# Kernel optimization log

Hardware: AMD Instinct MI355X
Metric: run time of the kernel (lower is better)

## Reference

```python
import jax, jax.numpy as jnp
import numpy as np

D_MODEL = 1024
N_HEADS = 16
D_HEAD = D_MODEL // N_HEADS


def setup_inputs() -> dict:
    key = jax.random.key(0)
    ks = jax.random.split(key, 11)
    B, S = 4, 2048
    scale = 1.0 / np.sqrt(D_MODEL)
    inp = {
        "query": jax.random.normal(ks[0], (B, S, D_MODEL), jnp.float32),
        "key": jax.random.normal(ks[1], (B, S, D_MODEL), jnp.float32),
        "value": jax.random.normal(ks[2], (B, S, D_MODEL), jnp.float32),
        "Wq": jax.random.normal(ks[3], (D_MODEL, D_MODEL), jnp.float32) * scale,
        "bq": jnp.zeros((D_MODEL,), jnp.float32),
        "Wk": jax.random.normal(ks[4], (D_MODEL, D_MODEL), jnp.float32) * scale,
        "bk": jnp.zeros((D_MODEL,), jnp.float32),
        "Wv": jax.random.normal(ks[5], (D_MODEL, D_MODEL), jnp.float32) * scale,
        "bv": jnp.zeros((D_MODEL,), jnp.float32),
        "Wo": jax.random.normal(ks[6], (D_MODEL, D_MODEL), jnp.float32) * scale,
        "bo": jnp.zeros((D_MODEL,), jnp.float32),
    }
    return inp


def _split_heads(x):
    b, s, _ = x.shape
    return x.reshape(b, s, N_HEADS, D_HEAD).transpose(0, 2, 1, 3)  # [b,h,s,dh]


def reference(query, key, value, Wq, bq, Wk, bk, Wv, bv, Wo, bo):
    Q = _split_heads(query @ Wq + bq)
    K = _split_heads(key @ Wk + bk)
    V = _split_heads(value @ Wv + bv)
    scores = jnp.einsum("bhqd,bhkd->bhqk", Q, K) / jnp.sqrt(jnp.float32(D_HEAD))
    attn = jax.nn.softmax(scores, axis=-1)  # dropout p=0 (eval)
    context = jnp.einsum("bhqk,bhkd->bhqd", attn, V)
    b, h, s, dh = context.shape
    context = context.transpose(0, 2, 1, 3).reshape(b, s, D_MODEL)
    return context @ Wo + bo
```

## Files before the change

kernel.cpp:

```cpp
#include <hip/hip_runtime.h>
#include <stdint.h>

#define DM 1024
#define SEQ 2048
#define MTOT 8192

typedef __attribute__((ext_vector_type(8))) short bf16x8;
typedef __attribute__((ext_vector_type(4))) float f32x4;
typedef __attribute__((ext_vector_type(16))) float f32x16;
typedef __attribute__((ext_vector_type(8))) unsigned short u16x8;
typedef __attribute__((ext_vector_type(4))) unsigned short u16x4;
typedef __attribute__((ext_vector_type(4))) uint32_t u32x4;
typedef __attribute__((ext_vector_type(2))) unsigned int u32x2;

__device__ __forceinline__ unsigned short f2bf(float x) {
  uint32_t u = __builtin_bit_cast(uint32_t, x);
  u += 0x7fffu + ((u >> 16) & 1u);
  return (unsigned short)(u >> 16);
}

__device__ __forceinline__ uint32_t cvtpk_bf16(float lo, float hi) {
  uint32_t r;
  asm("v_cvt_pk_bf16_f32 %0, %1, %2" : "=v"(r) : "v"(lo), "v"(hi));
  return r;
}

__device__ __forceinline__ void gload16(void* lds, const void* g) {
  __builtin_amdgcn_global_load_lds(
      (const __attribute__((address_space(1))) void*)(uintptr_t)g,
      (__attribute__((address_space(3))) void*)(uintptr_t)lds,
      16, 0, 0);
}

__global__ __launch_bounds__(256)
void prep_w(const float* __restrict__ w0, const float* __restrict__ w1,
            const float* __restrict__ w2, const float* __restrict__ w3,
            unsigned short* __restrict__ Wt) {
  const int z = blockIdx.z;
  const float* W = z == 0 ? w0 : z == 1 ? w1 : z == 2 ? w2 : w3;
  unsigned short* out = Wt + (size_t)z * 1048576;
  __shared__ float tile[32][33];
  const int n0 = blockIdx.x * 32, k0 = blockIdx.y * 32;
  const int tx = threadIdx.x & 31, ty = threadIdx.x >> 5;
#pragma unroll
  for (int j = 0; j < 32; j += 8)
    tile[ty + j][tx] = W[(size_t)(k0 + ty + j) * DM + n0 + tx];
  __syncthreads();
#pragma unroll
  for (int j = 0; j < 32; j += 8)
    out[(size_t)(n0 + ty + j) * DM + k0 + tx] = f2bf(tile[tx][ty + j]);
}

__global__ __launch_bounds__(256)
void cvt3(const float* __restrict__ q, const float* __restrict__ k,
          const float* __restrict__ v, unsigned short* __restrict__ out) {
  const int z = blockIdx.y;
  const float* in = z == 0 ? q : z == 1 ? k : v;
  unsigned short* o = out + (size_t)z * MTOT * DM;
  int i = blockIdx.x * 256 + threadIdx.x;
  f32x4 a = *(const f32x4*)(in + (size_t)i * 8);
  f32x4 b = *(const f32x4*)(in + (size_t)i * 8 + 4);
  u16x8 ov;
#pragma unroll
  for (int j = 0; j < 4; ++j) { ov[j] = f2bf(a[j]); ov[4 + j] = f2bf(b[j]); }
  *(u16x8*)(o + (size_t)i * 8) = ov;
}

template <int MODE>
__global__ __launch_bounds__(256)
void gemm_bt(const unsigned short* __restrict__ A,
             const unsigned short* __restrict__ Wt,
             const float* __restrict__ bias,
             void* __restrict__ C, float oscale) {
  __shared__ char sA[16384];
  __shared__ char sB[16384];
  const int t = threadIdx.x, wave = t >> 6, lane = t & 63;
  const int m0 = blockIdx.x * 128, n0 = blockIdx.y * 128;
  const int wr = (wave >> 1) * 64, wc = (wave & 1) * 64;
  const int lr = lane & 15, kg = lane >> 4;

  f32x4 acc[4][4];
#pragma unroll
  for (int i = 0; i < 4; ++i)
#pragma unroll
    for (int j = 0; j < 4; ++j) acc[i][j] = (f32x4){0.f, 0.f, 0.f, 0.f};

  for (int kt = 0; kt < 16; ++kt) {
    __syncthreads();
#pragma unroll
    for (int i = 0; i < 4; ++i) {
      int c = wave * 4 + i;
      int row = c * 8 + (lane >> 3);
      int bo = ((lane & 7) * 16) ^ ((row & 7) << 4);
      gload16(&sA[c * 1024], (const char*)(A + (size_t)(m0 + row) * DM + kt * 64) + bo);
      gload16(&sB[c * 1024], (const char*)(Wt + (size_t)(n0 + row) * DM + kt * 64) + bo);
    }
    __syncthreads();
#pragma unroll
    for (int ks = 0; ks < 2; ++ks) {
      bf16x8 afr[4], bfr[4];
#pragma unroll
      for (int j = 0; j < 4; ++j) {
        int mr = wr + j * 16 + lr;
        afr[j] = *(const bf16x8*)&sA[mr * 128 + ((ks * 64 + kg * 16) ^ ((mr & 7) << 4))];
        int nr = wc + j * 16 + lr;
        bfr[j] = *(const bf16x8*)&sB[nr * 128 + ((ks * 64 + kg * 16) ^ ((nr & 7) << 4))];
      }
#pragma unroll
      for (int mi = 0; mi < 4; ++mi)
#pragma unroll
        for (int nj = 0; nj < 4; ++nj)
          acc[mi][nj] = __builtin_amdgcn_mfma_f32_16x16x32_bf16(afr[mi], bfr[nj], acc[mi][nj], 0, 0, 0);
    }
  }
#pragma unroll
  for (int nj = 0; nj < 4; ++nj) {
    int col = n0 + wc + nj * 16 + lr;
    float bv = bias[col];
#pragma unroll
    for (int mi = 0; mi < 4; ++mi) {
      int rowseq = m0 + wr + mi * 16 + kg * 4;
      if (MODE == 2) {
        u16x4 pk;
#pragma unroll
        for (int r = 0; r < 4; ++r) pk[r] = f2bf(acc[mi][nj][r] + bv);
        *(u16x4*)((unsigned short*)C +
                  ((size_t)((rowseq >> 11) << 10) + col) * SEQ + (rowseq & 2047)) = pk;
      } else {
#pragma unroll
        for (int r = 0; r < 4; ++r) {
          float v = (acc[mi][nj][r] + bv) * oscale;
          if (MODE == 1) ((float*)C)[(size_t)(rowseq + r) * DM + col] = v;
          else ((unsigned short*)C)[(size_t)(rowseq + r) * DM + col] = f2bf(v);
        }
      }
    }
  }
}

__global__ __launch_bounds__(256)
void gemm_qkv(const unsigned short* __restrict__ Xall,
              const unsigned short* __restrict__ Wt,
              const float* __restrict__ bq, const float* __restrict__ bk,
              const float* __restrict__ bv,
              unsigned short* __restrict__ Qb, unsigned short* __restrict__ Kb,
              unsigned short* __restrict__ Vt, float qscale) {
  __shared__ char sA[16384];
  __shared__ char sB[16384];
  const int z = blockIdx.z;
  const unsigned short* A = Xall + (size_t)z * MTOT * DM;
  const unsigned short* W = Wt + (size_t)z * 1048576;
  const float* bias = z == 0 ? bq : z == 1 ? bk : bv;
  const int t = threadIdx.x, wave = t >> 6, lane = t & 63;
  const int m0 = blockIdx.x * 128, n0 = blockIdx.y * 128;
  const int wr = (wave >> 1) * 64, wc = (wave & 1) * 64;
  const int lr = lane & 15, kg = lane >> 4;

  f32x4 acc[4][4];
#pragma unroll
  for (int i = 0; i < 4; ++i)
#pragma unroll
    for (int j = 0; j < 4; ++j) acc[i][j] = (f32x4){0.f, 0.f, 0.f, 0.f};

  for (int kt = 0; kt < 16; ++kt) {
    __syncthreads();
#pragma unroll
    for (int i = 0; i < 4; ++i) {
      int c = wave * 4 + i;
      int row = c * 8 + (lane >> 3);
      int bo = ((lane & 7) * 16) ^ ((row & 7) << 4);
      gload16(&sA[c * 1024], (const char*)(A + (size_t)(m0 + row) * DM + kt * 64) + bo);
      gload16(&sB[c * 1024], (const char*)(W + (size_t)(n0 + row) * DM + kt * 64) + bo);
    }
    __syncthreads();
#pragma unroll
    for (int ks = 0; ks < 2; ++ks) {
      bf16x8 afr[4], bfr[4];
#pragma unroll
      for (int j = 0; j < 4; ++j) {
        int mr = wr + j * 16 + lr;
        afr[j] = *(const bf16x8*)&sA[mr * 128 + ((ks * 64 + kg * 16) ^ ((mr & 7) << 4))];
        int nr = wc + j * 16 + lr;
        bfr[j] = *(const bf16x8*)&sB[nr * 128 + ((ks * 64 + kg * 16) ^ ((nr & 7) << 4))];
      }
#pragma unroll
      for (int mi = 0; mi < 4; ++mi)
#pragma unroll
        for (int nj = 0; nj < 4; ++nj)
          acc[mi][nj] = __builtin_amdgcn_mfma_f32_16x16x32_bf16(afr[mi], bfr[nj], acc[mi][nj], 0, 0, 0);
    }
  }
  const float sc = z == 0 ? qscale : 1.0f;
#pragma unroll
  for (int nj = 0; nj < 4; ++nj) {
    int col = n0 + wc + nj * 16 + lr;
    float bvv = bias[col];
#pragma unroll
    for (int mi = 0; mi < 4; ++mi) {
      int rowseq = m0 + wr + mi * 16 + kg * 4;
      if (z == 2) {
        u16x4 pk;
#pragma unroll
        for (int r = 0; r < 4; ++r) pk[r] = f2bf(acc[mi][nj][r] + bvv);
        *(u16x4*)(Vt + ((size_t)((rowseq >> 11) << 10) + col) * SEQ + (rowseq & 2047)) = pk;
      } else {
        unsigned short* out = z == 0 ? Qb : Kb;
#pragma unroll
        for (int r = 0; r < 4; ++r)
          out[(size_t)(rowseq + r) * DM + col] = f2bf((acc[mi][nj][r] + bvv) * sc);
      }
    }
  }
}

__global__ __launch_bounds__(512)
void attn(const unsigned short* __restrict__ Qb,
          const unsigned short* __restrict__ Kb,
          const unsigned short* __restrict__ Vt,
          unsigned short* __restrict__ Ctx) {
  __shared__ char sK[4][8192];
  __shared__ char sV[4][8192];
  const int t = threadIdx.x, wave = t >> 6, lane = t & 63;
  const int l31 = lane & 31, hi = lane >> 5;
  const int bh = blockIdx.x, b = bh >> 4, h = bh & 15;
  const int q0 = blockIdx.y * 512;

  const int srow = wave * 8 + (lane >> 3);
  const int sbo = ((lane & 7) * 16) ^ ((srow & 7) << 4);
  const char* gK = (const char*)Kb + ((size_t)b * SEQ + srow) * (DM * 2) + h * 128 + sbo;
  const char* gV = (const char*)Vt + ((size_t)bh * 64 + srow) * (SEQ * 2) + sbo;

#define STAGE1(buf, kt) do { \
    gload16(&sK[buf][wave * 1024], gK + (size_t)(kt) * 131072); \
    gload16(&sV[buf][wave * 1024], gV + (size_t)(kt) * 128); \
  } while (0)

  bf16x8 qfA[4], qfB[4];
  {
    const unsigned short* qpA = Qb + ((size_t)b * SEQ + q0 + wave * 64 + l31) * DM + h * 64 + hi * 8;
    const unsigned short* qpB = qpA + (size_t)32 * DM;
#pragma unroll
    for (int ks = 0; ks < 4; ++ks) {
      qfA[ks] = *(const bf16x8*)(qpA + ks * 16);
      qfB[ks] = *(const bf16x8*)(qpB + ks * 16);
    }
  }

  f32x16 oA0, oA1, oB0, oB1, mInit;
#pragma unroll
  for (int i = 0; i < 16; ++i) {
    oA0[i] = 0.f; oA1[i] = 0.f; oB0[i] = 0.f; oB1[i] = 0.f; mInit[i] = -12.0f;
  }
  float lA = 0.f, lB = 0.f;

  STAGE1(0, 0);
  STAGE1(1, 1);
  __syncthreads();

  for (int p = 0; p < SEQ / 128; ++p) {
    if (p + 1 < SEQ / 128) {
      const int nt = 2 * p + 2;
      STAGE1(nt & 3, nt);
      STAGE1((nt + 1) & 3, nt + 1);
    }
#pragma unroll
    for (int half = 0; half < 2; ++half) {
      const int buf = 2 * (p & 1) + half;

      f32x16 sA0 = mInit, sA1 = mInit, sB0 = mInit, sB1 = mInit;
      const char* kbase = sK[buf];
      __builtin_amdgcn_s_setprio(1);
#pragma unroll
      for (int ks = 0; ks < 4; ++ks) {
        const int swz = (ks * 32 + hi * 16) ^ ((l31 & 7) << 4);
        bf16x8 kf0 = *(const bf16x8*)(kbase + l31 * 128 + swz);
        bf16x8 kf1 = *(const bf16x8*)(kbase + (32 + l31) * 128 + swz);
        sA0 = __builtin_amdgcn_mfma_f32_32x32x16_bf16(kf0, qfA[ks], sA0, 0, 0, 0);
        sB0 = __builtin_amdgcn_mfma_f32_32x32x16_bf16(kf0, qfB[ks], sB0, 0, 0, 0);
        sA1 = __builtin_amdgcn_mfma_f32_32x32x16_bf16(kf1, qfA[ks], sA1, 0, 0, 0);
        sB1 = __builtin_amdgcn_mfma_f32_32x32x16_bf16(kf1, qfB[ks], sB1, 0, 0, 0);
      }
      __builtin_amdgcn_s_setprio(0);

      {
        float a0 = 0.f, a1 = 0.f, b0 = 0.f, b1 = 0.f;
#pragma unroll
        for (int i = 0; i < 16; i += 2) {
          float pa0 = __builtin_amdgcn_exp2f(sA0[i + 0]); sA0[i + 0] = pa0; a0 += pa0;
          float pa1 = __builtin_amdgcn_exp2f(sA0[i + 1]); sA0[i + 1] = pa1; a1 += pa1;
          float pb0 = __builtin_amdgcn_exp2f(sB0[i + 0]); sB0[i + 0] = pb0; b0 += pb0;
          float pb1 = __builtin_amdgcn_exp2f(sB0[i + 1]); sB0[i + 1] = pb1; b1 += pb1;
        }
#pragma unroll
        for (int i = 0; i < 16; i += 2) {
          float pa0 = __builtin_amdgcn_exp2f(sA1[i + 0]); sA1[i + 0] = pa0; a0 += pa0;
          float pa1 = __builtin_amdgcn_exp2f(sA1[i + 1]); sA1[i + 1] = pa1; a1 += pa1;
          float pb0 = __builtin_amdgcn_exp2f(sB1[i + 0]); sB1[i + 0] = pb0; b0 += pb0;
          float pb1 = __builtin_amdgcn_exp2f(sB1[i + 1]); sB1[i + 1] = pb1; b1 += pb1;
        }
        lA += a0 + a1;
        lB += b0 + b1;
      }

      const char* vbase = sV[buf];
#pragma unroll
      for (int sl = 0; sl < 4; ++sl) {
        const f32x16& spA = (sl < 2) ? sA0 : sA1;
        const f32x16& spB = (sl < 2) ? sB0 : sB1;
        const int s8 = (sl & 1) * 8;
        uint32_t ax0 = cvtpk_bf16(spA[s8 + 0], spA[s8 + 1]);
        uint32_t ax1 = cvtpk_bf16(spA[s8 + 2], spA[s8 + 3]);
        uint32_t ay0 = cvtpk_bf16(spA[s8 + 4], spA[s8 + 5]);
        uint32_t ay1 = cvtpk_bf16(spA[s8 + 6], spA[s8 + 7]);
        u32x2 ra0 = __builtin_amdgcn_permlane32_swap(ax0, ay0, false, false);
        u32x2 ra1 = __builtin_amdgcn_permlane32_swap(ax1, ay1, false, false);
        u32x4 wvA;
        wvA[0] = ra0[0];
        wvA[1] = ra1[0];
        wvA[2] = ra0[1];
        wvA[3] = ra1[1];
        bf16x8 pfA = __builtin_bit_cast(bf16x8, wvA);
        uint32_t bx0 = cvtpk_bf16(spB[s8 + 0], spB[s8 + 1]);
        uint32_t bx1 = cvtpk_bf16(spB[s8 + 2], spB[s8 + 3]);
        uint32_t by0 = cvtpk_bf16(spB[s8 + 4], spB[s8 + 5]);
        uint32_t by1 = cvtpk_bf16(spB[s8 + 6], spB[s8 + 7]);
        u32x2 rb0 = __builtin_amdgcn_permlane32_swap(bx0, by0, false, false);
        u32x2 rb1 = __builtin_amdgcn_permlane32_swap(bx1, by1, false, false);
        u32x4 wvB;
        wvB[0] = rb0[0];
        wvB[1] = rb1[0];
        wvB[2] = rb0[1];
        wvB[3] = rb1[1];
        bf16x8 pfB = __builtin_bit_cast(bf16x8, wvB);

        const int swz = (sl * 32 + hi * 16) ^ ((l31 & 7) << 4);
        bf16x8 vf0 = *(const bf16x8*)(vbase + l31 * 128 + swz);
        bf16x8 vf1 = *(const bf16x8*)(vbase + (32 + l31) * 128 + swz);
        __builtin_amdgcn_s_setprio(1);
        oA0 = __builtin_amdgcn_mfma_f32_32x32x16_bf16(vf0, pfA, oA0, 0, 0, 0);
        oB0 = __builtin_amdgcn_mfma_f32_32x32x16_bf16(vf0, pfB, oB0, 0, 0, 0);
        oA1 = __builtin_amdgcn_mfma_f32_32x32x16_bf16(vf1, pfA, oA1, 0, 0, 0);
        oB1 = __builtin_amdgcn_mfma_f32_32x32x16_bf16(vf1, pfB, oB1, 0, 0, 0);
        __builtin_amdgcn_s_setprio(0);
      }
    }
    __syncthreads();
  }
#undef STAGE1

  float ltA = lA + __shfl_xor(lA, 32);
  float ltB = lB + __shfl_xor(lB, 32);
  float invA = 1.0f / ltA, invB = 1.0f / ltB;
  unsigned short* orowA = Ctx + ((size_t)b * SEQ + q0 + wave * 64 + l31) * DM + h * 64;
  unsigned short* orowB = orowA + (size_t)32 * DM;
#pragma unroll
  for (int dt = 0; dt < 2; ++dt) {
    const f32x16& oa = dt ? oA1 : oA0;
    const f32x16& ob = dt ? oB1 : oB0;
#pragma unroll
    for (int rg = 0; rg < 4; ++rg) {
      u16x4 pkA, pkB;
#pragma unroll
      for (int i = 0; i < 4; ++i) {
        pkA[i] = f2bf(oa[rg * 4 + i] * invA);
        pkB[i] = f2bf(ob[rg * 4 + i] * invB);
      }
      *(u16x4*)(orowA + dt * 32 + rg * 8 + hi * 4) = pkA;
      *(u16x4*)(orowB + dt * 32 + rg * 8 + hi * 4) = pkB;
    }
  }
}

extern "C" void kernel_launch(void* const* d_in, const int* in_sizes, int n_in,
                              void* d_out, int out_size, void* d_ws, size_t ws_size,
                              hipStream_t stream) {
  const float* query = (const float*)d_in[0];
  const float* key   = (const float*)d_in[1];
  const float* value = (const float*)d_in[2];
  const float* Wq = (const float*)d_in[3];
  const float* bq = (const float*)d_in[4];
  const float* Wk = (const float*)d_in[5];
  const float* bk = (const float*)d_in[6];
  const float* Wv = (const float*)d_in[7];
  const float* bv = (const float*)d_in[8];
  const float* Wo = (const float*)d_in[9];
  const float* bo = (const float*)d_in[10];

  const float QSCALE = 0.125f * 1.44269504088896340736f;
  char* ws = (char*)d_ws;
  const size_t MB = 1048576;

  prep_w<<<dim3(32, 32, 4), 256, 0, stream>>>(Wq, Wk, Wv, Wo, (unsigned short*)ws);
  unsigned short* Wt = (unsigned short*)ws;

  if (ws_size >= 104 * MB) {
    unsigned short* Xall = (unsigned short*)(ws + 8 * MB);
    unsigned short* Qb   = (unsigned short*)(ws + 56 * MB);
    unsigned short* Kb   = (unsigned short*)(ws + 72 * MB);
    unsigned short* Vt   = (unsigned short*)(ws + 88 * MB);
    unsigned short* Xc   = Xall;

    cvt3<<<dim3(4096, 3), 256, 0, stream>>>(query, key, value, Xall);
    gemm_qkv<<<dim3(64, 8, 3), 256, 0, stream>>>(Xall, Wt, bq, bk, bv,
                                                 Qb, Kb, Vt, QSCALE);
    attn<<<dim3(64, 4), 512, 0, stream>>>(Qb, Kb, Vt, Xc);
    gemm_bt<1><<<dim3(64, 8), 256, 0, stream>>>(Xc, Wt + (size_t)3 * 1048576, bo, d_out, 1.0f);
  } else {
    unsigned short* Qb = (unsigned short*)(ws + 8 * MB);
    unsigned short* Kb = (unsigned short*)(ws + 24 * MB);
    unsigned short* Vt = (unsigned short*)(ws + 40 * MB);
    unsigned short* Xc = (unsigned short*)(ws + 56 * MB);

    cvt3<<<dim3(4096, 1), 256, 0, stream>>>(query, query, query, Xc);
    gemm_bt<0><<<dim3(64, 8), 256, 0, stream>>>(Xc, Wt, bq, Qb, QSCALE);
    cvt3<<<dim3(4096, 1), 256, 0, stream>>>(key, key, key, Xc);
    gemm_bt<0><<<dim3(64, 8), 256, 0, stream>>>(Xc, Wt + (size_t)1048576, bk, Kb, 1.0f);
    cvt3<<<dim3(4096, 1), 256, 0, stream>>>(value, value, value, Xc);
    gemm_bt<2><<<dim3(64, 8), 256, 0, stream>>>(Xc, Wt + (size_t)2 * 1048576, bv, Vt, 1.0f);
    attn<<<dim3(64, 4), 512, 0, stream>>>(Qb, Kb, Vt, Xc);
    gemm_bt<1><<<dim3(64, 8), 256, 0, stream>>>(Xc, Wt + (size_t)3 * 1048576, bo, d_out, 1.0f);
  }
}
```

Before: 190.6 us.

## Split attention KV range across two blocks and merge partial outputs

```diff
diff --git a/kernel.cpp b/kernel.cpp
--- a/kernel.cpp
+++ b/kernel.cpp
@@ -17,6 +17,11 @@
   uint32_t u = __builtin_bit_cast(uint32_t, x);
   u += 0x7fffu + ((u >> 16) & 1u);
   return (unsigned short)(u >> 16);
+}
+
+__device__ __forceinline__ float bf2f(unsigned short x) {
+  uint32_t u = (uint32_t)x << 16;
+  return __builtin_bit_cast(float, u);
 }
 
 __device__ __forceinline__ uint32_t cvtpk_bf16(float lo, float hi) {
@@ -217,13 +222,18 @@
 void attn(const unsigned short* __restrict__ Qb,
           const unsigned short* __restrict__ Kb,
           const unsigned short* __restrict__ Vt,
-          unsigned short* __restrict__ Ctx) {
+          unsigned short* __restrict__ Ctx,
+          float* __restrict__ Lpart,
+          int split) {
   __shared__ char sK[4][8192];
   __shared__ char sV[4][8192];
   const int t = threadIdx.x, wave = t >> 6, lane = t & 63;
   const int l31 = lane & 31, hi = lane >> 5;
   const int bh = blockIdx.x, b = bh >> 4, h = bh & 15;
   const int q0 = blockIdx.y * 512;
+  const int z = blockIdx.z;
+  const int ktb = z * 16;
+  const int ntp = split ? 8 : 16;
 
   const int srow = wave * 8 + (lane >> 3);
   const int sbo = ((lane & 7) * 16) ^ ((srow & 7) << 4);
@@ -253,15 +263,15 @@
   }
   float lA = 0.f, lB = 0.f;
 
-  STAGE1(0, 0);
-  STAGE1(1, 1);
+  STAGE1(0, ktb + 0);
+  STAGE1(1, ktb + 1);
   __syncthreads();
 
-  for (int p = 0; p < SEQ / 128; ++p) {
-    if (p + 1 < SEQ / 128) {
+  for (int p = 0; p < ntp; ++p) {
+    if (p + 1 < ntp) {
       const int nt = 2 * p + 2;
-      STAGE1(nt & 3, nt);
-      STAGE1((nt + 1) & 3, nt + 1);
+      STAGE1(nt & 3, ktb + nt);
+      STAGE1((nt + 1) & 3, ktb + nt + 1);
     }
 #pragma unroll
     for (int half = 0; half < 2; ++half) {
@@ -350,8 +360,10 @@
 
   float ltA = lA + __shfl_xor(lA, 32);
   float ltB = lB + __shfl_xor(lB, 32);
-  float invA = 1.0f / ltA, invB = 1.0f / ltB;
-  unsigned short* orowA = Ctx + ((size_t)b * SEQ + q0 + wave * 64 + l31) * DM + h * 64;
+  float invA = split ? 1.0f : 1.0f / ltA;
+  float invB = split ? 1.0f : 1.0f / ltB;
+  unsigned short* obase = Ctx + (size_t)z * (split ? (size_t)MTOT * DM : 0);
+  unsigned short* orowA = obase + ((size_t)b * SEQ + q0 + wave * 64 + l31) * DM + h * 64;
   unsigned short* orowB = orowA + (size_t)32 * DM;
 #pragma unroll
   for (int dt = 0; dt < 2; ++dt) {
@@ -369,6 +381,31 @@
       *(u16x4*)(orowB + dt * 32 + rg * 8 + hi * 4) = pkB;
     }
   }
+  if (split && hi == 0) {
+    float* Lrow = Lpart + (size_t)z * 131072 + (size_t)bh * SEQ + q0 + wave * 64;
+    Lrow[l31] = ltA;
+    Lrow[32 + l31] = ltB;
+  }
+}
+
+__global__ __launch_bounds__(256)
+void merge_o(const unsigned short* __restrict__ O0,
+             const unsigned short* __restrict__ O1,
+             const float* __restrict__ L,
+             unsigned short* __restrict__ Xc) {
+  int g = blockIdx.x * 256 + threadIdx.x;
+  int srow = g >> 7, c8 = (g & 127) << 3;
+  int h = c8 >> 6;
+  int b = srow >> 11, q = srow & 2047;
+  size_t li = (size_t)(b * 16 + h) * SEQ + q;
+  float inv = 1.0f / (L[li] + L[131072 + li]);
+  u16x8 a = *(const u16x8*)(O0 + (size_t)srow * DM + c8);
+  u16x8 bb = *(const u16x8*)(O1 + (size_t)srow * DM + c8);
+  u16x8 o;
+#pragma unroll
+  for (int j = 0; j < 8; ++j)
+    o[j] = f2bf((bf2f(a[j]) + bf2f(bb[j])) * inv);
+  *(u16x8*)(Xc + (size_t)srow * DM + c8) = o;
 }
 
 extern "C" void kernel_launch(void* const* d_in, const int* in_sizes, int n_in,
@@ -398,12 +435,16 @@
     unsigned short* Qb   = (unsigned short*)(ws + 56 * MB);
     unsigned short* Kb   = (unsigned short*)(ws + 72 * MB);
     unsigned short* Vt   = (unsigned short*)(ws + 88 * MB);
-    unsigned short* Xc   = Xall;
+    unsigned short* Op0  = (unsigned short*)(ws + 8 * MB);
+    unsigned short* Op1  = (unsigned short*)(ws + 24 * MB);
+    unsigned short* Xc   = (unsigned short*)(ws + 40 * MB);
+    float* Lpart         = (float*)ws;
 
     cvt3<<<dim3(4096, 3), 256, 0, stream>>>(query, key, value, Xall);
     gemm_qkv<<<dim3(64, 8, 3), 256, 0, stream>>>(Xall, Wt, bq, bk, bv,
                                                  Qb, Kb, Vt, QSCALE);
-    attn<<<dim3(64, 4), 512, 0, stream>>>(Qb, Kb, Vt, Xc);
+    attn<<<dim3(64, 4, 2), 512, 0, stream>>>(Qb, Kb, Vt, Op0, Lpart, 1);
+    merge_o<<<4096, 256, 0, stream>>>(Op0, Op1, Lpart, Xc);
     gemm_bt<1><<<dim3(64, 8), 256, 0, stream>>>(Xc, Wt + (size_t)3 * 1048576, bo, d_out, 1.0f);
   } else {
     unsigned short* Qb = (unsigned short*)(ws + 8 * MB);
@@ -417,7 +458,7 @@
     gemm_bt<0><<<dim3(64, 8), 256, 0, stream>>>(Xc, Wt + (size_t)1048576, bk, Kb, 1.0f);
     cvt3<<<dim3(4096, 1), 256, 0, stream>>>(value, value, value, Xc);
     gemm_bt<2><<<dim3(64, 8), 256, 0, stream>>>(Xc, Wt + (size_t)2 * 1048576, bv, Vt, 1.0f);
-    attn<<<dim3(64, 4), 512, 0, stream>>>(Qb, Kb, Vt, Xc);
+    attn<<<dim3(64, 4, 1), 512, 0, stream>>>(Qb, Kb, Vt, Xc, nullptr, 0);
     gemm_bt<1><<<dim3(64, 8), 256, 0, stream>>>(Xc, Wt + (size_t)3 * 1048576, bo, d_out, 1.0f);
   }
 }
```

Measured after the change: 209.2 us, median of 2. 9.8% more time.
